# Performance work log

Measured on AMD Instinct MI355X. Metric: run time of the kernel, lower is better.

## Reference

```python
import jax, jax.numpy as jnp
import numpy as np

B, N, D, NH, L, DFF = 2, 2048, 256, 8, 4, 1024
DH = D // NH
FACTOR = 0.5 / float(np.sqrt(DH))  # == 1/sqrt(4*DH), matches q/k feature dim 4*d_head
EPS = 1e-5


def _ln(x, g, b):
    m = x.mean(-1, keepdims=True)
    v = ((x - m) ** 2).mean(-1, keepdims=True)
    return (x - m) * jax.lax.rsqrt(v + EPS) * g + b


def setup_inputs() -> dict:
    key = jax.random.key(0)
    ks = jax.random.split(key, 16)
    s = 0.05
    r = lambda i, shape: jax.random.normal(ks[i], shape, dtype=jnp.float32)
    return {
        "H": r(0, (B, N, D)),
        "V": r(1, (B, N, 3, D)),
        "D_batch": r(2, (B, N, N)),
        "rbf_feat": r(3, (L, B, 1, N, N)),
        "H_mask": jnp.ones((B, N), dtype=bool),
        "ln1_g": jnp.ones((L, D)), "ln1_b": jnp.zeros((L, D)),
        "ln2_g": jnp.ones((L, D)), "ln2_b": jnp.zeros((L, D)),
        "Wq": r(4, (L, D, 4 * D)) * s, "bq": jnp.zeros((L, 4 * D)),
        "Wk": r(5, (L, D, 4 * D)) * s, "bk": jnp.zeros((L, 4 * D)),
        "Wv": r(6, (L, D, D)) * s, "bv": jnp.zeros((L, D)),
        "Wvv": r(7, (L, D, D)) * s,
        "Wo": r(8, (L, D, D)) * s, "bo": jnp.zeros((L, D)),
        "Wvo": r(9, (L, D, D)) * s,
        "Wlv": r(10, (L, D, 2 * D)) * s,
        "W1": r(11, (L, 2 * D, DFF)) * s, "b1": jnp.zeros((L, DFF)),
        "W2": r(12, (L, DFF, 2 * D)) * s, "b2": jnp.zeros((L, 2 * D)),
    }


def _stack_forward(H, V, D_batch, rbf_feat, H_mask, ln1_g, ln1_b, ln2_g, ln2_b,
                   Wq, bq, Wk, bk, Wv, bv, Wvv, Wo, bo, Wvo, Wlv, W1, b1, W2, b2):
    b, n = H.shape[:2]
    mask = H_mask[:, None, None, :]       # [B,1,1,N] masks key columns
    base_bias = D_batch[:, None]          # [B,1,N,N]

    def step(carry, xs):
        H, V = carry
        (rbf, g1, be1, g2, be2, wq, bq_, wk, bk_, wv, bv_, wvv,
         wo, bo_, wvo, wlv, w1, b1_, w2, b2_) = xs
        # --- self-attention sublayer (pre-LN on scalar stream only) ---
        Hn = _ln(H, g1, be1)
        Hq = (Hn @ wq + bq_).reshape(b, n, NH, 4 * DH)
        Hk = (Hn @ wk + bk_).reshape(b, n, NH, 4 * DH)
        Hv = (Hn @ wv + bv_).reshape(b, n, NH, DH)
        Vv = (V @ wvv).reshape(b, n, 3, NH, DH)
        Vv = jnp.swapaxes(Vv, 2, 3).reshape(b, n, NH, 3 * DH)
        V_attn = jnp.concatenate([Hv, Vv], axis=-1)        # [B,N,H,4*DH]
        bias = jnp.where(mask, rbf + base_bias, -jnp.inf)  # [B,1,N,N]
        scores = jnp.einsum('bnhd,bmhd->bhnm', Hq, Hk) * FACTOR + bias
        attn = jax.nn.softmax(scores, axis=-1)
        res = jnp.einsum('bhnm,bmhd->bnhd', attn, V_attn)  # [B,N,H,4*DH]
        H_res = res[..., :DH].reshape(b, n, D)
        V_res = jnp.swapaxes(res[..., DH:].reshape(b, n, NH, 3, DH), 2, 3).reshape(b, n, 3, D)
        H = H + (H_res @ wo + bo_)
        V = V + V_res @ wvo
        # --- GVP FFN sublayer (pre-LN on scalar stream only) ---
        Hn = _ln(H, g2, be2)
        Vp = V @ wlv                                       # [B,N,3,2D]
        V1, V2 = Vp[..., :D], Vp[..., D:]
        scaler = jnp.concatenate([Hn, jnp.linalg.norm(V1, axis=-2)], axis=-1)
        sc = jax.nn.silu(scaler @ w1 + b1_) @ w2 + b2_
        H = H + sc[..., :D]
        V = V + sc[..., D:][..., None, :] * V2             # vector_act='none'
        return (H, V), None

    xs = (rbf_feat, ln1_g, ln1_b, ln2_g, ln2_b, Wq, bq, Wk, bk, Wv, bv, Wvv,
          Wo, bo, Wvo, Wlv, W1, b1, W2, b2)
    (H, V), _ = jax.lax.scan(step, (H, V), xs)
    return H, V


def reference(H, V, D_batch, rbf_feat, H_mask, ln1_g, ln1_b, ln2_g, ln2_b,
              Wq, bq, Wk, bk, Wv, bv, Wvv, Wo, bo, Wvo, Wlv, W1, b1, W2, b2):
    return _stack_forward(H, V, D_batch, rbf_feat, H_mask, ln1_g, ln1_b, ln2_g, ln2_b,
                          Wq, bq, Wk, bk, Wv, bv, Wvv, Wo, bo, Wvo, Wlv, W1, b1, W2, b2)
```

## Files before the change

### kernel.cpp

```cpp
#include <hip/hip_runtime.h>
#include <math.h>

static constexpr int B_  = 2;
static constexpr int N_  = 2048;
static constexpr int D_  = 256;
static constexpr int NH_ = 8;
static constexpr int L_  = 4;
static constexpr int DH_ = 32;
static constexpr int DQ_ = 128;
static constexpr float FACTOR_ = 0.08838834764831845f;
static constexpr float EPS_ = 1e-5f;

typedef short    short8   __attribute__((ext_vector_type(8)));
typedef unsigned short us4 __attribute__((ext_vector_type(4)));
typedef unsigned short us8 __attribute__((ext_vector_type(8)));
typedef float    f32x4    __attribute__((ext_vector_type(4)));
typedef unsigned short us;

__device__ __forceinline__ us f2b(float f) {
  unsigned u = __float_as_uint(f);
  unsigned r = u + 0x7FFF + ((u >> 16) & 1);
  return (us)(r >> 16);
}
__device__ __forceinline__ float b2f(us u) {
  return __uint_as_float(((unsigned)u) << 16);
}
__device__ __forceinline__ void gl_lds16(const void* g, void* l) {
  __builtin_amdgcn_global_load_lds(
      (const __attribute__((address_space(1))) void*)g,
      (__attribute__((address_space(3))) void*)l, 16, 0, 0);
}

__global__ __launch_bounds__(256) void ln_kernel(const float* __restrict__ X,
    const float* __restrict__ g, const float* __restrict__ b,
    us* __restrict__ Y) {
  __shared__ float r1[256], r2[256];
  int row = blockIdx.x, tid = threadIdx.x;
  float x = X[(size_t)row * D_ + tid];
  r1[tid] = x; r2[tid] = x * x;
  __syncthreads();
  for (int s = 128; s > 0; s >>= 1) {
    if (tid < s) { r1[tid] += r1[tid + s]; r2[tid] += r2[tid + s]; }
    __syncthreads();
  }
  float mean = r1[0] * (1.0f / D_);
  float var  = r2[0] * (1.0f / D_) - mean * mean;
  float inv  = rsqrtf(var + EPS_);
  Y[(size_t)row * D_ + tid] = f2b((x - mean) * inv * g[tid] + b[tid]);
}

__global__ __launch_bounds__(256) void conv_bf16(const float* __restrict__ X,
    us* __restrict__ Y) {
  size_t i = ((size_t)blockIdx.x * 256 + threadIdx.x) * 4;
  float4 v = *(const float4*)&X[i];
  us4 o = { f2b(v.x), f2b(v.y), f2b(v.z), f2b(v.w) };
  *(us4*)&Y[i] = o;
}

__global__ __launch_bounds__(256) void biascomb(const float* __restrict__ R,
    const float* __restrict__ Dq, us* __restrict__ Out) {
  size_t i = ((size_t)blockIdx.x * 256 + threadIdx.x) * 8;
  float4 r0 = *(const float4*)&R[i];
  float4 r1 = *(const float4*)&R[i + 4];
  float4 d0 = *(const float4*)&Dq[i];
  float4 d1 = *(const float4*)&Dq[i + 4];
  us8 o = { f2b(r0.x + d0.x), f2b(r0.y + d0.y), f2b(r0.z + d0.z), f2b(r0.w + d0.w),
            f2b(r1.x + d1.x), f2b(r1.y + d1.y), f2b(r1.z + d1.z), f2b(r1.w + d1.w) };
  *(us8*)&Out[i] = o;
}

struct WConvDesc {
  const float* src[9];
  unsigned dst[9];
  int K[9];
  int N[9];
  int start[10];
};
__global__ __launch_bounds__(256) void wconv_kernel(WConvDesc d, us* __restrict__ Wb) {
  __shared__ float T[64][65];
  int bid = blockIdx.x, tid = threadIdx.x;
  int j = 0;
  #pragma unroll
  for (int q = 0; q < 8; q++) if (bid >= d.start[q + 1]) j = q + 1;
  int t = bid - d.start[j];
  int K = d.K[j], N = d.N[j];
  int tpr = N >> 6;
  int tk = t / tpr, tn = t - tk * tpr;
  const float* src = d.src[j];
  us* dst = Wb + d.dst[j];
  #pragma unroll
  for (int i = 0; i < 4; i++) {
    int r = i * 16 + (tid >> 4), c = (tid & 15) * 4;
    *(float4*)&T[r][c] = *(const float4*)&src[(size_t)(tk * 64 + r) * N + tn * 64 + c];
  }
  __syncthreads();
  #pragma unroll
  for (int i = 0; i < 4; i++) {
    int n = i * 16 + (tid >> 4), k = (tid & 15) * 4;
    us4 o = { f2b(T[k][n]), f2b(T[k + 1][n]), f2b(T[k + 2][n]), f2b(T[k + 3][n]) };
    *(us4*)&dst[(size_t)(tn * 64 + n) * K + tk * 64 + k] = o;
  }
}

template<int BIG, int BIAS, int ACC, int SILU, int WF, int WB, int QK>
__global__ __launch_bounds__(256, 2) void gemm_v2(const us* __restrict__ A,
    const us* __restrict__ Wt, const float* __restrict__ bias,
    const float* __restrict__ bias2, float* __restrict__ Cf, us* __restrict__ Cb,
    int M, int K, int Nc, float oscale) {
  constexpr int BM  = BIG ? 128 : 64;
  constexpr int NF  = BIG ? 4 : 2;
  constexpr int WS  = NF * 16;
  constexpr int NLD = BM / 32;
  __shared__ us As[2][BM * 64];
  __shared__ us Bs[2][BM * 64];
  const int tid = threadIdx.x;
  const int w = tid >> 6, l = tid & 63;
  const int lx = l & 15, ly = l >> 4;
  const int wr = w >> 1, wc = w & 1;
  const int bn = blockIdx.x, bm = blockIdx.y;
  const int swz = (lx & 7) << 4;
  const char* Ag = (const char*)A + (size_t)(bm * BM) * K * 2;
  const char* Bg = (const char*)Wt + (size_t)(bn * BM) * K * 2;
  const size_t rowb = (size_t)K * 2;

  #define GSTAGE(buf, k0)                                                     \
    do {                                                                      \
      _Pragma("unroll")                                                       \
      for (int j = 0; j < NLD; j++) {                                         \
        int o = j * 4096 + tid * 16;                                          \
        int r = o >> 7, cb = o & 127;                                         \
        int sc = cb ^ ((r & 7) << 4);                                         \
        gl_lds16(Ag + (size_t)r * rowb + (size_t)(k0) * 2 + sc,               \
                 &As[buf][(j * 4096 + w * 1024) >> 1]);                       \
        gl_lds16(Bg + (size_t)r * rowb + (size_t)(k0) * 2 + sc,               \
                 &Bs[buf][(j * 4096 + w * 1024) >> 1]);                       \
      }                                                                       \
    } while (0)

  f32x4 acc[NF][NF];
  #pragma unroll
  for (int i = 0; i < NF; i++)
    #pragma unroll
    for (int j = 0; j < NF; j++) acc[i][j] = (f32x4){0.f, 0.f, 0.f, 0.f};

  int cur = 0;
  GSTAGE(0, 0);
  __syncthreads();
  for (int k0 = 0; k0 < K; k0 += 64) {
    if (k0 + 64 < K) GSTAGE(cur ^ 1, k0 + 64);
    #pragma unroll
    for (int s = 0; s < 2; s++) {
      short8 af[NF], bf[NF];
      #pragma unroll
      for (int mt = 0; mt < NF; mt++)
        af[mt] = *(const short8*)
            &As[cur][(((wr * WS + mt * 16 + lx) * 128) + ((s * 64 + ly * 16) ^ swz)) >> 1];
      #pragma unroll
      for (int nt = 0; nt < NF; nt++)
        bf[nt] = *(const short8*)
            &Bs[cur][(((wc * WS + nt * 16 + lx) * 128) + ((s * 64 + ly * 16) ^ swz)) >> 1];
      __builtin_amdgcn_s_setprio(1);
      #pragma unroll
      for (int mt = 0; mt < NF; mt++)
        #pragma unroll
        for (int nt = 0; nt < NF; nt++)
          acc[mt][nt] = __builtin_amdgcn_mfma_f32_16x16x32_bf16(af[mt], bf[nt], acc[mt][nt], 0, 0, 0);
      __builtin_amdgcn_s_setprio(0);
    }
    __syncthreads();
    cur ^= 1;
  }
  #undef GSTAGE

  #pragma unroll
  for (int nt = 0; nt < NF; nt++) {
    const int n = bn * BM + wc * WS + nt * 16 + lx;
    float bval = 0.f, osc = oscale;
    if (QK) {
      bval = (n < 1024) ? bias[n] : bias2[n - 1024];
      osc = (n < 1024) ? oscale : 1.0f;
    } else if (BIAS) {
      bval = bias[n];
    }
    #pragma unroll
    for (int mt = 0; mt < NF; mt++) {
      #pragma unroll
      for (int r = 0; r < 4; r++) {
        const int m = bm * BM + wr * WS + mt * 16 + ly * 4 + r;
        float v = acc[mt][nt][r] + bval;
        if (SILU) v = v / (1.f + __expf(-v));
        size_t idx = (size_t)m * Nc + n;
        if (ACC) v += Cf[idx];
        if (WF) Cf[idx] = v;
        if (WB) Cb[idx] = f2b(v * osc);
      }
    }
  }
}

__global__ __launch_bounds__(256) void pack_vattn_t(const us* __restrict__ Hv,
    const us* __restrict__ Vv, us* __restrict__ Vt) {
  __shared__ us T[64][136];
  const int bid = blockIdx.x;
  const int nt = bid & 31, hh = (bid >> 5) & 7, b = bid >> 8;
  const int n0 = nt * 64;
  const int tid = threadIdx.x;
  {
    const int nn = tid >> 2, part = tid & 3;
    const size_t row = (size_t)(b * N_ + n0 + nn);
    const us* src = (part == 0) ? (Hv + row * D_ + hh * DH_)
                                : (Vv + (row * 3 + (part - 1)) * D_ + hh * DH_);
    #pragma unroll
    for (int jj = 0; jj < 32; jj += 8)
      *(us8*)&T[nn][part * 32 + jj] = *(const us8*)(src + jj);
  }
  __syncthreads();
  const int d = tid >> 1, half = tid & 1;
  size_t ob = ((size_t)(b * NH_ + hh) * DQ_ + d) * (size_t)N_ + n0 + half * 32;
  #pragma unroll
  for (int i = 0; i < 32; i += 8) {
    us8 o;
    #pragma unroll
    for (int e = 0; e < 8; e++) o[e] = T[half * 32 + i + e][d];
    *(us8*)&Vt[ob + i] = o;
  }
}

__global__ __launch_bounds__(256, 2) void attn_mfma(
    const us* __restrict__ QKb,
    const us* __restrict__ Vtb,
    const us* __restrict__ bias,
    us* __restrict__ Hres,
    us* __restrict__ Vres) {
  __shared__ us Kt[2][8192];
  __shared__ us Vt[2][8192];
  __shared__ us Plds[4][16][72];
  const int bid = blockIdx.x;
  const int h  = bid >> 6;
  const int g  = bid & 63;
  const int b  = g >> 5;
  const int qt = g & 31;
  const int tid = threadIdx.x;
  const int w  = tid >> 6;
  const int l  = tid & 63;
  const int lx = l & 15;
  const int ly = l >> 4;
  const int qrow = qt * 64 + w * 16 + lx;
  const int swz = (lx & 7) << 4;

  short8 qf[4];
  {
    const us* qp = QKb + (size_t)(b * N_ + qrow) * 2048 + h * DQ_ + ly * 8;
    #pragma unroll
    for (int s = 0; s < 4; s++) qf[s] = *(const short8*)(qp + s * 32);
  }
  const char* kg = (const char*)QKb + (size_t)b * N_ * 4096 + 2048 + h * 256;
  const char* vg = (const char*)(Vtb + ((size_t)(b * NH_ + h) * DQ_) * (size_t)N_);
  const us* bbase = bias + ((size_t)b * N_ + qrow) * N_;

  #define STAGE(buf, m0)                                                      \
    do {                                                                      \
      _Pragma("unroll")                                                       \
      for (int j = 0; j < 4; j++) {                                           \
        int o = j * 4096 + tid * 16;                                          \
        int r = o >> 8, cb = o & 255;                                         \
        int scb = cb ^ ((r & 7) << 4);                                        \
        gl_lds16(kg + (size_t)((m0) + r) * 4096 + scb,                        \
                 &Kt[buf][(j * 4096 + w * 1024) >> 1]);                       \
      }                                                                       \
      _Pragma("unroll")                                                       \
      for (int j = 0; j < 4; j++) {                                           \
        int o = j * 4096 + tid * 16;                                          \
        int r = o >> 7, cb = o & 127;                                         \
        int scb = cb ^ ((r & 7) << 4);                                        \
        gl_lds16(vg + (size_t)r * (N_ * 2) + (size_t)(m0) * 2 + scb,          \
                 &Vt[buf][(j * 4096 + w * 1024) >> 1]);                       \
      }                                                                       \
    } while (0)

  float m_run = -3.0e38f, l_run = 0.f;
  f32x4 oacc[8];
  #pragma unroll
  for (int i = 0; i < 8; i++) oacc[i] = (f32x4){0.f, 0.f, 0.f, 0.f};

  int cur = 0;
  STAGE(0, 0);
  __syncthreads();

  for (int mc0 = 0; mc0 < N_; mc0 += 64) {
    if (mc0 + 64 < N_) STAGE(cur ^ 1, mc0 + 64);
    us4 bb[4];
    #pragma unroll
    for (int t = 0; t < 4; t++) bb[t] = *(const us4*)(bbase + mc0 + t * 16 + ly * 4);
    f32x4 sacc[4];
    #pragma unroll
    for (int t = 0; t < 4; t++) sacc[t] = (f32x4){0.f, 0.f, 0.f, 0.f};
    __builtin_amdgcn_s_setprio(1);
    #pragma unroll
    for (int t = 0; t < 4; t++) {
      #pragma unroll
      for (int s = 0; s < 4; s++) {
        const short8 kf = *(const short8*)
            &Kt[cur][((t * 16 + lx) * 256 + ((s * 64 + ly * 16) ^ swz)) >> 1];
        sacc[t] = __builtin_amdgcn_mfma_f32_16x16x32_bf16(kf, qf[s], sacc[t], 0, 0, 0);
      }
    }
    __builtin_amdgcn_s_setprio(0);
    float pvv[16];
    #pragma unroll
    for (int t = 0; t < 4; t++) {
      pvv[t*4+0] = sacc[t][0] + b2f(bb[t][0]);
      pvv[t*4+1] = sacc[t][1] + b2f(bb[t][1]);
      pvv[t*4+2] = sacc[t][2] + b2f(bb[t][2]);
      pvv[t*4+3] = sacc[t][3] + b2f(bb[t][3]);
    }
    float a8[8], a4[4];
    #pragma unroll
    for (int i = 0; i < 8; i++) a8[i] = fmaxf(pvv[i], pvv[i + 8]);
    #pragma unroll
    for (int i = 0; i < 4; i++) a4[i] = fmaxf(a8[i], a8[i + 4]);
    float mloc = fmaxf(fmaxf(a4[0], a4[1]), fmaxf(a4[2], a4[3]));
    mloc = fmaxf(mloc, __shfl_xor(mloc, 16, 64));
    mloc = fmaxf(mloc, __shfl_xor(mloc, 32, 64));
    float m_new = fmaxf(m_run, mloc);
    float scale = __expf(m_run - m_new);
    float s8[8], s4[4];
    #pragma unroll
    for (int i = 0; i < 16; i++) pvv[i] = __expf(pvv[i] - m_new);
    #pragma unroll
    for (int i = 0; i < 8; i++) s8[i] = pvv[i] + pvv[i + 8];
    #pragma unroll
    for (int i = 0; i < 4; i++) s4[i] = s8[i] + s8[i + 4];
    float lloc = (s4[0] + s4[1]) + (s4[2] + s4[3]);
    lloc += __shfl_xor(lloc, 16, 64);
    lloc += __shfl_xor(lloc, 32, 64);
    l_run = l_run * scale + lloc;
    m_run = m_new;
    #pragma unroll
    for (int i = 0; i < 8; i++) {
      oacc[i][0] *= scale; oacc[i][1] *= scale;
      oacc[i][2] *= scale; oacc[i][3] *= scale;
    }
    #pragma unroll
    for (int t = 0; t < 4; t++) {
      us4 pk = { f2b(pvv[t*4+0]), f2b(pvv[t*4+1]), f2b(pvv[t*4+2]), f2b(pvv[t*4+3]) };
      *(us4*)&Plds[w][lx][t * 16 + ly * 4] = pk;
    }
    short8 pf0 = *(const short8*)&Plds[w][lx][ly * 8];
    short8 pf1 = *(const short8*)&Plds[w][lx][32 + ly * 8];
    __builtin_amdgcn_s_setprio(1);
    #pragma unroll
    for (int dt = 0; dt < 8; dt++) {
      const int rb = (dt * 16 + lx) * 128;
      const short8 vf0 = *(const short8*)&Vt[cur][(rb + ((ly * 16) ^ swz)) >> 1];
      const short8 vf1 = *(const short8*)&Vt[cur][(rb + ((64 + ly * 16) ^ swz)) >> 1];
      oacc[dt] = __builtin_amdgcn_mfma_f32_16x16x32_bf16(vf0, pf0, oacc[dt], 0, 0, 0);
      oacc[dt] = __builtin_amdgcn_mfma_f32_16x16x32_bf16(vf1, pf1, oacc[dt], 0, 0, 0);
    }
    __builtin_amdgcn_s_setprio(0);
    __syncthreads();
    cur ^= 1;
  }
  #undef STAGE
  float inv = 1.0f / l_run;
  const size_t row = (size_t)(b * N_ + qrow);
  #pragma unroll
  for (int dt = 0; dt < 8; dt++) {
    const int d0 = dt * 16 + ly * 4;
    us4 pk = { f2b(oacc[dt][0] * inv), f2b(oacc[dt][1] * inv),
               f2b(oacc[dt][2] * inv), f2b(oacc[dt][3] * inv) };
    if (d0 < 32) {
      *(us4*)&Hres[row * D_ + h * DH_ + d0] = pk;
    } else {
      const int c = (d0 - DH_) >> 5, dd = (d0 - DH_) & 31;
      *(us4*)&Vres[(row * 3 + c) * D_ + h * DH_ + dd] = pk;
    }
  }
}

__global__ __launch_bounds__(256) void scaler_kernel(const us* __restrict__ Hn,
    const float* __restrict__ Vp, us* __restrict__ scal) {
  size_t row = blockIdx.x;
  int j = threadIdx.x;
  scal[row * 512 + j] = Hn[row * D_ + j];
  float a  = Vp[(row * 3 + 0) * 512 + j];
  float c1 = Vp[(row * 3 + 1) * 512 + j];
  float c2 = Vp[(row * 3 + 2) * 512 + j];
  scal[row * 512 + D_ + j] = f2b(sqrtf(a * a + c1 * c1 + c2 * c2));
}

__global__ __launch_bounds__(256) void final_update(float* __restrict__ H,
    float* __restrict__ V, const float* __restrict__ sc,
    const float* __restrict__ Vp, us* __restrict__ Vb) {
  size_t row = blockIdx.x;
  int j = threadIdx.x;
  H[row * D_ + j] += sc[row * 512 + j];
  float s = sc[row * 512 + D_ + j];
  #pragma unroll
  for (int c = 0; c < 3; c++) {
    size_t vi = (row * 3 + c) * D_ + j;
    float nv = V[vi] + s * Vp[(row * 3 + c) * 512 + D_ + j];
    V[vi] = nv;
    Vb[vi] = f2b(nv);
  }
}

extern "C" void kernel_launch(void* const* d_in, const int* in_sizes, int n_in,
                              void* d_out, int out_size, void* d_ws, size_t ws_size,
                              hipStream_t stream) {
  const float* H_in = (const float*)d_in[0];
  const float* V_in = (const float*)d_in[1];
  const float* Db   = (const float*)d_in[2];
  const float* rbf  = (const float*)d_in[3];
  const float* ln1g = (const float*)d_in[5];
  const float* ln1b = (const float*)d_in[6];
  const float* ln2g = (const float*)d_in[7];
  const float* ln2b = (const float*)d_in[8];
  const float* Wq  = (const float*)d_in[9];
  const float* bq  = (const float*)d_in[10];
  const float* Wk  = (const float*)d_in[11];
  const float* bk  = (const float*)d_in[12];
  const float* Wv  = (const float*)d_in[13];
  const float* bv  = (const float*)d_in[14];
  const float* Wvv = (const float*)d_in[15];
  const float* Wo  = (const float*)d_in[16];
  const float* bo  = (const float*)d_in[17];
  const float* Wvo = (const float*)d_in[18];
  const float* Wlv = (const float*)d_in[19];
  const float* W1  = (const float*)d_in[20];
  const float* b1  = (const float*)d_in[21];
  const float* W2  = (const float*)d_in[22];
  const float* b2  = (const float*)d_in[23];

  const size_t HN = (size_t)B_ * N_ * D_;
  const size_t VN = HN * 3;
  float* Hs = (float*)d_out;
  float* Vs = (float*)d_out + HN;
  float* ws = (float*)d_ws;
  us*    bias_b = (us*)ws;
  us*    Wb     = (us*)(ws + 4194304);
  us*    Vb     = (us*)(ws + 5177344);
  us*    Hnb    = (us*)(ws + 6750208);
  us*    QKb    = (us*)(ws + 7274496);
  us*    Vtb    = (us*)(ws + 11468800);
  us*    Hvb    = (us*)(ws + 13565952);
  us*    Vvb    = (us*)(ws + 14090240);
  us*    Hres_b = (us*)(ws + 6750208);
  us*    Vres_b = (us*)(ws + 13565952);
  us*    Hn2b   = (us*)(ws + 6750208);
  float* Vp     = ws + 7274496;
  us*    scal_b = (us*)(ws + 13565952);
  us*    midb   = (us*)(ws + 15014528);
  float* scb    = ws;

  hipMemcpyAsync(Hs, H_in, HN * sizeof(float), hipMemcpyDeviceToDevice, stream);
  hipMemcpyAsync(Vs, V_in, VN * sizeof(float), hipMemcpyDeviceToDevice, stream);
  conv_bf16<<<3072, 256, 0, stream>>>(V_in, Vb);

  const int ROWS  = B_ * N_;
  static const int wKs[9] = {256,256,256,256,256,256,256,512,1024};
  static const int wNs[9] = {1024,1024,256,256,256,256,512,1024,512};
  static const unsigned wOff[9] = {0,262144,524288,589824,655360,720896,786432,917504,1441792};
  static const int wStart[10] = {0,64,128,144,160,176,192,224,352,480};

  for (int l = 0; l < L_; ++l) {
    WConvDesc dsc;
    const float* srcs[9] = {
      Wq  + (size_t)l * 256 * 1024, Wk  + (size_t)l * 256 * 1024,
      Wv  + (size_t)l * 256 * 256,  Wvv + (size_t)l * 256 * 256,
      Wo  + (size_t)l * 256 * 256,  Wvo + (size_t)l * 256 * 256,
      Wlv + (size_t)l * 256 * 512,  W1  + (size_t)l * 512 * 1024,
      W2  + (size_t)l * 1024 * 512 };
    for (int j = 0; j < 9; j++) {
      dsc.src[j] = srcs[j]; dsc.dst[j] = wOff[j];
      dsc.K[j] = wKs[j]; dsc.N[j] = wNs[j]; dsc.start[j] = wStart[j];
    }
    dsc.start[9] = wStart[9];
    wconv_kernel<<<480, 256, 0, stream>>>(dsc, Wb);
    biascomb<<<4096, 256, 0, stream>>>(rbf + (size_t)l * B_ * N_ * N_, Db, bias_b);

    ln_kernel<<<ROWS, 256, 0, stream>>>(Hs, ln1g + l * D_, ln1b + l * D_, Hnb);
    gemm_v2<1,1,0,0,0,1,1><<<dim3(16, 32), 256, 0, stream>>>(
        Hnb, Wb + wOff[0], bq + l * 1024, bk + l * 1024, nullptr, QKb, 4096, 256, 2048, FACTOR_);
    gemm_v2<0,1,0,0,0,1,0><<<dim3(4, 64), 256, 0, stream>>>(
        Hnb, Wb + wOff[2], bv + l * 256, nullptr, nullptr, Hvb, 4096, 256, 256, 1.f);
    gemm_v2<0,0,0,0,0,1,0><<<dim3(4, 192), 256, 0, stream>>>(
        Vb, Wb + wOff[3], nullptr, nullptr, nullptr, Vvb, 12288, 256, 256, 1.f);
    pack_vattn_t<<<512, 256, 0, stream>>>(Hvb, Vvb, Vtb);
    attn_mfma<<<512, 256, 0, stream>>>(QKb, Vtb, bias_b, Hres_b, Vres_b);
    gemm_v2<0,1,1,0,1,0,0><<<dim3(4, 64), 256, 0, stream>>>(
        Hres_b, Wb + wOff[4], bo + l * 256, nullptr, Hs, nullptr, 4096, 256, 256, 1.f);
    gemm_v2<0,0,1,0,1,1,0><<<dim3(4, 192), 256, 0, stream>>>(
        Vres_b, Wb + wOff[5], nullptr, nullptr, Vs, Vb, 12288, 256, 256, 1.f);
    ln_kernel<<<ROWS, 256, 0, stream>>>(Hs, ln2g + l * D_, ln2b + l * D_, Hn2b);
    gemm_v2<0,0,0,0,1,0,0><<<dim3(8, 192), 256, 0, stream>>>(
        Vb, Wb + wOff[6], nullptr, nullptr, Vp, nullptr, 12288, 256, 512, 1.f);
    scaler_kernel<<<ROWS, 256, 0, stream>>>(Hn2b, Vp, scal_b);
    gemm_v2<1,1,0,1,0,1,0><<<dim3(8, 32), 256, 0, stream>>>(
        scal_b, Wb + wOff[7], b1 + l * 1024, nullptr, nullptr, midb, 4096, 512, 1024, 1.f);
    gemm_v2<0,1,0,0,1,0,0><<<dim3(8, 64), 256, 0, stream>>>(
        midb, Wb + wOff[8], b2 + l * 512, nullptr, scb, nullptr, 4096, 1024, 512, 1.f);
    final_update<<<ROWS, 256, 0, stream>>>(Hs, Vs, scb, Vp, Vb);
  }
}
```

Measured before the change: 857.0 us.

## Fuse bias combine into attention, register-staged KV, lazy softmax rescale, fuse layernorms

Removes the separate biascomb pass. Attention now reads fp32 rbf and distance directly and adds them in registers. K/V staging changes from double-buffered direct-to-LDS loads to register prefetch into a single LDS buffer, and launch bounds are raised to 4 to allow more resident blocks. Softmax rescaling is skipped unless the running max grows by more than 8, and the P tile in LDS is swizzled. The second layernorm is fused into the scaler kernel and the next layer's first layernorm into the final update, which trades extra fp32 bias reads inside attention for fewer launches and less intermediate traffic.

```diff
diff --git a/kernel.cpp b/kernel.cpp
--- a/kernel.cpp
+++ b/kernel.cpp
@@ -55,18 +55,6 @@
   float4 v = *(const float4*)&X[i];
   us4 o = { f2b(v.x), f2b(v.y), f2b(v.z), f2b(v.w) };
   *(us4*)&Y[i] = o;
-}
-
-__global__ __launch_bounds__(256) void biascomb(const float* __restrict__ R,
-    const float* __restrict__ Dq, us* __restrict__ Out) {
-  size_t i = ((size_t)blockIdx.x * 256 + threadIdx.x) * 8;
-  float4 r0 = *(const float4*)&R[i];
-  float4 r1 = *(const float4*)&R[i + 4];
-  float4 d0 = *(const float4*)&Dq[i];
-  float4 d1 = *(const float4*)&Dq[i + 4];
-  us8 o = { f2b(r0.x + d0.x), f2b(r0.y + d0.y), f2b(r0.z + d0.z), f2b(r0.w + d0.w),
-            f2b(r1.x + d1.x), f2b(r1.y + d1.y), f2b(r1.z + d1.z), f2b(r1.w + d1.w) };
-  *(us8*)&Out[i] = o;
 }
 
 struct WConvDesc {
@@ -226,15 +214,16 @@
   }
 }
 
-__global__ __launch_bounds__(256, 2) void attn_mfma(
+__global__ __launch_bounds__(256, 4) void attn_mfma(
     const us* __restrict__ QKb,
     const us* __restrict__ Vtb,
-    const us* __restrict__ bias,
+    const float* __restrict__ rbf,
+    const float* __restrict__ Db,
     us* __restrict__ Hres,
     us* __restrict__ Vres) {
-  __shared__ us Kt[2][8192];
-  __shared__ us Vt[2][8192];
-  __shared__ us Plds[4][16][72];
+  __shared__ us Kt[8192];
+  __shared__ us Vt[8192];
+  __shared__ us Plds[4][16 * 64];
   const int bid = blockIdx.x;
   const int h  = bid >> 6;
   const int g  = bid & 63;
@@ -256,25 +245,29 @@
   }
   const char* kg = (const char*)QKb + (size_t)b * N_ * 4096 + 2048 + h * 256;
   const char* vg = (const char*)(Vtb + ((size_t)(b * NH_ + h) * DQ_) * (size_t)N_);
-  const us* bbase = bias + ((size_t)b * N_ + qrow) * N_;
-
-  #define STAGE(buf, m0)                                                      \
+  const float* rbase = rbf + ((size_t)b * N_ + qrow) * N_;
+  const float* dbase = Db  + ((size_t)b * N_ + qrow) * N_;
+
+  us8 kreg[4], vreg[4];
+  #define LOADKV(m0)                                                          \
     do {                                                                      \
       _Pragma("unroll")                                                       \
       for (int j = 0; j < 4; j++) {                                           \
         int o = j * 4096 + tid * 16;                                          \
-        int r = o >> 8, cb = o & 255;                                         \
-        int scb = cb ^ ((r & 7) << 4);                                        \
-        gl_lds16(kg + (size_t)((m0) + r) * 4096 + scb,                        \
-                 &Kt[buf][(j * 4096 + w * 1024) >> 1]);                       \
+        int rk = o >> 8, ck = o & 255;                                        \
+        kreg[j] = *(const us8*)(kg + (size_t)((m0) + rk) * 4096 +             \
+                                (ck ^ ((rk & 7) << 4)));                      \
+        int rv = o >> 7, cv = o & 127;                                        \
+        vreg[j] = *(const us8*)(vg + (size_t)rv * (N_ * 2) +                  \
+                                (size_t)(m0) * 2 + (cv ^ ((rv & 7) << 4)));   \
       }                                                                       \
+    } while (0)
+  #define WRITEKV()                                                           \
+    do {                                                                      \
       _Pragma("unroll")                                                       \
       for (int j = 0; j < 4; j++) {                                           \
-        int o = j * 4096 + tid * 16;                                          \
-        int r = o >> 7, cb = o & 127;                                         \
-        int scb = cb ^ ((r & 7) << 4);                                        \
-        gl_lds16(vg + (size_t)r * (N_ * 2) + (size_t)(m0) * 2 + scb,          \
-                 &Vt[buf][(j * 4096 + w * 1024) >> 1]);                       \
+        *(us8*)&Kt[j * 2048 + tid * 8] = kreg[j];                             \
+        *(us8*)&Vt[j * 2048 + tid * 8] = vreg[j];                             \
       }                                                                       \
     } while (0)
 
@@ -283,15 +276,18 @@
   #pragma unroll
   for (int i = 0; i < 8; i++) oacc[i] = (f32x4){0.f, 0.f, 0.f, 0.f};
 
-  int cur = 0;
-  STAGE(0, 0);
+  LOADKV(0);
+  WRITEKV();
+  LOADKV(64);
   __syncthreads();
 
   for (int mc0 = 0; mc0 < N_; mc0 += 64) {
-    if (mc0 + 64 < N_) STAGE(cur ^ 1, mc0 + 64);
-    us4 bb[4];
-    #pragma unroll
-    for (int t = 0; t < 4; t++) bb[t] = *(const us4*)(bbase + mc0 + t * 16 + ly * 4);
+    float4 r4[4], d4[4];
+    #pragma unroll
+    for (int t = 0; t < 4; t++) {
+      r4[t] = *(const float4*)(rbase + mc0 + t * 16 + ly * 4);
+      d4[t] = *(const float4*)(dbase + mc0 + t * 16 + ly * 4);
+    }
     f32x4 sacc[4];
     #pragma unroll
     for (int t = 0; t < 4; t++) sacc[t] = (f32x4){0.f, 0.f, 0.f, 0.f};
@@ -301,7 +297,7 @@
       #pragma unroll
       for (int s = 0; s < 4; s++) {
         const short8 kf = *(const short8*)
-            &Kt[cur][((t * 16 + lx) * 256 + ((s * 64 + ly * 16) ^ swz)) >> 1];
+            &Kt[((t * 16 + lx) * 256 + ((s * 64 + ly * 16) ^ swz)) >> 1];
         sacc[t] = __builtin_amdgcn_mfma_f32_16x16x32_bf16(kf, qf[s], sacc[t], 0, 0, 0);
       }
     }
@@ -309,10 +305,10 @@
     float pvv[16];
     #pragma unroll
     for (int t = 0; t < 4; t++) {
-      pvv[t*4+0] = sacc[t][0] + b2f(bb[t][0]);
-      pvv[t*4+1] = sacc[t][1] + b2f(bb[t][1]);
-      pvv[t*4+2] = sacc[t][2] + b2f(bb[t][2]);
-      pvv[t*4+3] = sacc[t][3] + b2f(bb[t][3]);
+      pvv[t*4+0] = sacc[t][0] + r4[t].x + d4[t].x;
+      pvv[t*4+1] = sacc[t][1] + r4[t].y + d4[t].y;
+      pvv[t*4+2] = sacc[t][2] + r4[t].z + d4[t].z;
+      pvv[t*4+3] = sacc[t][3] + r4[t].w + d4[t].w;
     }
     float a8[8], a4[4];
     #pragma unroll
@@ -322,11 +318,20 @@
     float mloc = fmaxf(fmaxf(a4[0], a4[1]), fmaxf(a4[2], a4[3]));
     mloc = fmaxf(mloc, __shfl_xor(mloc, 16, 64));
     mloc = fmaxf(mloc, __shfl_xor(mloc, 32, 64));
-    float m_new = fmaxf(m_run, mloc);
-    float scale = __expf(m_run - m_new);
+    if (!__all(mloc - m_run <= 8.0f)) {
+      float m_new = fmaxf(m_run, mloc);
+      float scale = __expf(m_run - m_new);
+      l_run *= scale;
+      #pragma unroll
+      for (int i = 0; i < 8; i++) {
+        oacc[i][0] *= scale; oacc[i][1] *= scale;
+        oacc[i][2] *= scale; oacc[i][3] *= scale;
+      }
+      m_run = m_new;
+    }
     float s8[8], s4[4];
     #pragma unroll
-    for (int i = 0; i < 16; i++) pvv[i] = __expf(pvv[i] - m_new);
+    for (int i = 0; i < 16; i++) pvv[i] = __expf(pvv[i] - m_run);
     #pragma unroll
     for (int i = 0; i < 8; i++) s8[i] = pvv[i] + pvv[i + 8];
     #pragma unroll
@@ -334,34 +339,33 @@
     float lloc = (s4[0] + s4[1]) + (s4[2] + s4[3]);
     lloc += __shfl_xor(lloc, 16, 64);
     lloc += __shfl_xor(lloc, 32, 64);
-    l_run = l_run * scale + lloc;
-    m_run = m_new;
-    #pragma unroll
-    for (int i = 0; i < 8; i++) {
-      oacc[i][0] *= scale; oacc[i][1] *= scale;
-      oacc[i][2] *= scale; oacc[i][3] *= scale;
-    }
+    l_run += lloc;
     #pragma unroll
     for (int t = 0; t < 4; t++) {
       us4 pk = { f2b(pvv[t*4+0]), f2b(pvv[t*4+1]), f2b(pvv[t*4+2]), f2b(pvv[t*4+3]) };
-      *(us4*)&Plds[w][lx][t * 16 + ly * 4] = pk;
-    }
-    short8 pf0 = *(const short8*)&Plds[w][lx][ly * 8];
-    short8 pf1 = *(const short8*)&Plds[w][lx][32 + ly * 8];
+      *(us4*)((char*)&Plds[w][0] + lx * 128 + ((t * 32 + ly * 8) ^ swz)) = pk;
+    }
+    short8 pf0 = *(const short8*)((const char*)&Plds[w][0] + lx * 128 + ((ly * 16) ^ swz));
+    short8 pf1 = *(const short8*)((const char*)&Plds[w][0] + lx * 128 + ((64 + ly * 16) ^ swz));
     __builtin_amdgcn_s_setprio(1);
     #pragma unroll
     for (int dt = 0; dt < 8; dt++) {
       const int rb = (dt * 16 + lx) * 128;
-      const short8 vf0 = *(const short8*)&Vt[cur][(rb + ((ly * 16) ^ swz)) >> 1];
-      const short8 vf1 = *(const short8*)&Vt[cur][(rb + ((64 + ly * 16) ^ swz)) >> 1];
+      const short8 vf0 = *(const short8*)&Vt[(rb + ((ly * 16) ^ swz)) >> 1];
+      const short8 vf1 = *(const short8*)&Vt[(rb + ((64 + ly * 16) ^ swz)) >> 1];
       oacc[dt] = __builtin_amdgcn_mfma_f32_16x16x32_bf16(vf0, pf0, oacc[dt], 0, 0, 0);
       oacc[dt] = __builtin_amdgcn_mfma_f32_16x16x32_bf16(vf1, pf1, oacc[dt], 0, 0, 0);
     }
     __builtin_amdgcn_s_setprio(0);
     __syncthreads();
-    cur ^= 1;
-  }
-  #undef STAGE
+    if (mc0 + 64 < N_) {
+      WRITEKV();
+      if (mc0 + 128 < N_) LOADKV(mc0 + 128);
+      __syncthreads();
+    }
+  }
+  #undef LOADKV
+  #undef WRITEKV
   float inv = 1.0f / l_run;
   const size_t row = (size_t)(b * N_ + qrow);
   #pragma unroll
@@ -378,23 +382,39 @@
   }
 }
 
-__global__ __launch_bounds__(256) void scaler_kernel(const us* __restrict__ Hn,
+__global__ __launch_bounds__(256) void ln2scaler(const float* __restrict__ H,
+    const float* __restrict__ g, const float* __restrict__ b,
     const float* __restrict__ Vp, us* __restrict__ scal) {
+  __shared__ float r1[256], r2[256];
   size_t row = blockIdx.x;
   int j = threadIdx.x;
-  scal[row * 512 + j] = Hn[row * D_ + j];
+  float x = H[row * D_ + j];
+  r1[j] = x; r2[j] = x * x;
+  __syncthreads();
+  for (int s = 128; s > 0; s >>= 1) {
+    if (j < s) { r1[j] += r1[j + s]; r2[j] += r2[j + s]; }
+    __syncthreads();
+  }
+  float mean = r1[0] * (1.0f / D_);
+  float var  = r2[0] * (1.0f / D_) - mean * mean;
+  float inv  = rsqrtf(var + EPS_);
+  scal[row * 512 + j] = f2b((x - mean) * inv * g[j] + b[j]);
   float a  = Vp[(row * 3 + 0) * 512 + j];
   float c1 = Vp[(row * 3 + 1) * 512 + j];
   float c2 = Vp[(row * 3 + 2) * 512 + j];
   scal[row * 512 + D_ + j] = f2b(sqrtf(a * a + c1 * c1 + c2 * c2));
 }
 
-__global__ __launch_bounds__(256) void final_update(float* __restrict__ H,
+__global__ __launch_bounds__(256) void final_ln(float* __restrict__ H,
     float* __restrict__ V, const float* __restrict__ sc,
-    const float* __restrict__ Vp, us* __restrict__ Vb) {
+    const float* __restrict__ Vp, us* __restrict__ Vb,
+    const float* __restrict__ g, const float* __restrict__ b,
+    us* __restrict__ Hnb) {
+  __shared__ float r1[256], r2[256];
   size_t row = blockIdx.x;
   int j = threadIdx.x;
-  H[row * D_ + j] += sc[row * 512 + j];
+  float hnew = H[row * D_ + j] + sc[row * 512 + j];
+  H[row * D_ + j] = hnew;
   float s = sc[row * 512 + D_ + j];
   #pragma unroll
   for (int c = 0; c < 3; c++) {
@@ -402,6 +422,18 @@
     float nv = V[vi] + s * Vp[(row * 3 + c) * 512 + D_ + j];
     V[vi] = nv;
     Vb[vi] = f2b(nv);
+  }
+  if (g) {
+    r1[j] = hnew; r2[j] = hnew * hnew;
+    __syncthreads();
+    for (int st = 128; st > 0; st >>= 1) {
+      if (j < st) { r1[j] += r1[j + st]; r2[j] += r2[j + st]; }
+      __syncthreads();
+    }
+    float mean = r1[0] * (1.0f / D_);
+    float var  = r2[0] * (1.0f / D_) - mean * mean;
+    float inv  = rsqrtf(var + EPS_);
+    Hnb[row * D_ + j] = f2b((hnew - mean) * inv * g[j] + b[j]);
   }
 }
 
@@ -437,7 +469,6 @@
   float* Hs = (float*)d_out;
   float* Vs = (float*)d_out + HN;
   float* ws = (float*)d_ws;
-  us*    bias_b = (us*)ws;
   us*    Wb     = (us*)(ws + 4194304);
   us*    Vb     = (us*)(ws + 5177344);
   us*    Hnb    = (us*)(ws + 6750208);
@@ -447,7 +478,6 @@
   us*    Vvb    = (us*)(ws + 14090240);
   us*    Hres_b = (us*)(ws + 6750208);
   us*    Vres_b = (us*)(ws + 13565952);
-  us*    Hn2b   = (us*)(ws + 6750208);
   float* Vp     = ws + 7274496;
   us*    scal_b = (us*)(ws + 13565952);
   us*    midb   = (us*)(ws + 15014528);
@@ -477,9 +507,9 @@
     }
     dsc.start[9] = wStart[9];
     wconv_kernel<<<480, 256, 0, stream>>>(dsc, Wb);
-    biascomb<<<4096, 256, 0, stream>>>(rbf + (size_t)l * B_ * N_ * N_, Db, bias_b);
-
-    ln_kernel<<<ROWS, 256, 0, stream>>>(Hs, ln1g + l * D_, ln1b + l * D_, Hnb);
+    if (l == 0)
+      ln_kernel<<<ROWS, 256, 0, stream>>>(Hs, ln1g, ln1b, Hnb);
+
     gemm_v2<1,1,0,0,0,1,1><<<dim3(16, 32), 256, 0, stream>>>(
         Hnb, Wb + wOff[0], bq + l * 1024, bk + l * 1024, nullptr, QKb, 4096, 256, 2048, FACTOR_);
     gemm_v2<0,1,0,0,0,1,0><<<dim3(4, 64), 256, 0, stream>>>(
@@ -487,19 +517,21 @@
     gemm_v2<0,0,0,0,0,1,0><<<dim3(4, 192), 256, 0, stream>>>(
         Vb, Wb + wOff[3], nullptr, nullptr, nullptr, Vvb, 12288, 256, 256, 1.f);
     pack_vattn_t<<<512, 256, 0, stream>>>(Hvb, Vvb, Vtb);
-    attn_mfma<<<512, 256, 0, stream>>>(QKb, Vtb, bias_b, Hres_b, Vres_b);
+    attn_mfma<<<512, 256, 0, stream>>>(QKb, Vtb,
+        rbf + (size_t)l * B_ * N_ * N_, Db, Hres_b, Vres_b);
     gemm_v2<0,1,1,0,1,0,0><<<dim3(4, 64), 256, 0, stream>>>(
         Hres_b, Wb + wOff[4], bo + l * 256, nullptr, Hs, nullptr, 4096, 256, 256, 1.f);
     gemm_v2<0,0,1,0,1,1,0><<<dim3(4, 192), 256, 0, stream>>>(
         Vres_b, Wb + wOff[5], nullptr, nullptr, Vs, Vb, 12288, 256, 256, 1.f);
-    ln_kernel<<<ROWS, 256, 0, stream>>>(Hs, ln2g + l * D_, ln2b + l * D_, Hn2b);
     gemm_v2<0,0,0,0,1,0,0><<<dim3(8, 192), 256, 0, stream>>>(
         Vb, Wb + wOff[6], nullptr, nullptr, Vp, nullptr, 12288, 256, 512, 1.f);
-    scaler_kernel<<<ROWS, 256, 0, stream>>>(Hn2b, Vp, scal_b);
+    ln2scaler<<<ROWS, 256, 0, stream>>>(Hs, ln2g + l * D_, ln2b + l * D_, Vp, scal_b);
     gemm_v2<1,1,0,1,0,1,0><<<dim3(8, 32), 256, 0, stream>>>(
         scal_b, Wb + wOff[7], b1 + l * 1024, nullptr, nullptr, midb, 4096, 512, 1024, 1.f);
     gemm_v2<0,1,0,0,1,0,0><<<dim3(8, 64), 256, 0, stream>>>(
         midb, Wb + wOff[8], b2 + l * 512, nullptr, scb, nullptr, 4096, 1024, 512, 1.f);
-    final_update<<<ROWS, 256, 0, stream>>>(Hs, Vs, scb, Vp, Vb);
-  }
-}
+    final_ln<<<ROWS, 256, 0, stream>>>(Hs, Vs, scb, Vp, Vb,
+        (l < 3) ? (ln1g + (l + 1) * D_) : nullptr,
+        (l < 3) ? (ln1b + (l + 1) * D_) : nullptr, Hnb);
+  }
+}
```

Result: slower. 1.748 ms (+103.9%).
